# Performance work log

Hardware: AMD Instinct MI355X
Metric: run time of the kernel (lower is better)

The kernel has to match this reference:

```python
import jax, jax.numpy as jnp
import numpy as np

B, N, E, F, D = 8, 2000, 64000, 1024, 128
NEG_SLOPE = 0.01  # torch LeakyReLU default

def leaky(x):
    return jnp.where(x >= 0, x, NEG_SLOPE * x)

def gcn_conv(x, ei, W, b):
    # PyG GCNConv: add self loops, symmetric norm, x @ W, scatter-sum, + bias
    src, tgt = ei[0], ei[1]
    loops = jnp.arange(N, dtype=src.dtype)
    src_a = jnp.concatenate([src, loops])
    tgt_a = jnp.concatenate([tgt, loops])
    deg = jax.ops.segment_sum(jnp.ones(src_a.shape, x.dtype), tgt_a, num_segments=N)
    dinv = jnp.where(deg > 0, jax.lax.rsqrt(deg), 0.0)
    norm = dinv[src_a] * dinv[tgt_a]  # [E+N]
    h = x @ W                          # [N, F]
    out = jax.ops.segment_sum(norm[:, None] * h[src_a], tgt_a, num_segments=N)
    return out + b

gcn_conv_b = jax.vmap(gcn_conv, in_axes=(0, 0, None, None))

def setup_inputs() -> dict:
    key = jax.random.key(0)
    ks = jax.random.split(key, 16)
    s = lambda fan: 1.0 / np.sqrt(fan)
    return {
        "x1": jax.random.normal(ks[0], (B, N, F), jnp.float32),
        "ei1": jax.random.randint(ks[1], (B, 2, E), 0, N, jnp.int32),
        "x2": jax.random.normal(ks[2], (B, N, F), jnp.float32),
        "ei2": jax.random.randint(ks[3], (B, 2, E), 0, N, jnp.int32),
        "Wg1": jax.random.normal(ks[4], (F, F), jnp.float32) * s(F),
        "bg1": jnp.zeros((F,), jnp.float32),
        "Wf1": jax.random.normal(ks[5], (F, D), jnp.float32) * s(F),
        "bf1": jnp.zeros((D,), jnp.float32),
        "Wg2": jax.random.normal(ks[6], (F, F), jnp.float32) * s(F),
        "bg2": jnp.zeros((F,), jnp.float32),
        "Wf2": jax.random.normal(ks[7], (F, D), jnp.float32) * s(F),
        "bf2": jnp.zeros((D,), jnp.float32),
        "W1": jax.random.normal(ks[8], (2 * D, 256), jnp.float32) * s(2 * D),
        "b1": jnp.zeros((256,), jnp.float32),
        "W2": jax.random.normal(ks[9], (256, 64), jnp.float32) * s(256),
        "b2": jnp.zeros((64,), jnp.float32),
        "Wo": jax.random.normal(ks[10], (64, 1), jnp.float32) * s(64),
        "bo": jnp.zeros((1,), jnp.float32),
    }

def reference(x1, ei1, x2, ei2, Wg1, bg1, Wf1, bf1, Wg2, bg2, Wf2, bf2,
              W1, b1, W2, b2, Wo, bo):
    # branch 1
    h1 = leaky(gcn_conv_b(x1, ei1, Wg1, bg1))       # [B, N, F]
    g1 = jnp.mean(h1, axis=1)                        # [B, F]
    g1 = leaky(g1 @ Wf1 + bf1)                       # [B, D] (dropout = eval identity)
    # branch 2
    h2 = leaky(gcn_conv_b(x2, ei2, Wg2, bg2))
    g2 = jnp.mean(h2, axis=1)
    g2 = leaky(g2 @ Wf2 + bf2)
    # head
    xc = jnp.concatenate([g1, g2], axis=1)           # [B, 2D]
    xc = leaky(xc @ W1 + b1)
    xc = leaky(xc @ W2 + b2)
    return jax.nn.sigmoid(xc @ Wo + bo)              # [B, 1]
```

## Files before the change

### kernel.cpp

```cpp
#include <hip/hip_runtime.h>
#include <stdint.h>

#define B 8
#define NN 2000
#define EG 64000
#define FF 1024
#define DD 128
#define BK 32
#define NCHUNK 125

#define NB_CONV 32000
#define NB_WT   2048
#define NB_DEG  4000
#define NB_GEMMS 1024
#define NB_FILL  4000

typedef short short8 __attribute__((ext_vector_type(8)));
typedef float f32x4 __attribute__((ext_vector_type(4)));
typedef float f32x2 __attribute__((ext_vector_type(2)));

__device__ __forceinline__ unsigned short f2bf(float f) {
    union { float f; unsigned int u; } v; v.f = f;
    unsigned int u = v.u;
    unsigned int r = u + 0x7FFFu + ((u >> 16) & 1u);
    return (unsigned short)(r >> 16);
}
__device__ __forceinline__ float leaky(float v) { return v >= 0.0f ? v : 0.01f * v; }

__device__ __forceinline__ void acc8p(f32x2* __restrict__ r, float w, uint4 v) {
    union { unsigned int u; float f; } c;
    f32x2 wv = {w, w};
    f32x2 h;
    c.u = v.x << 16;          h.x = c.f;
    c.u = v.x & 0xffff0000u;  h.y = c.f;
    r[0] += wv * h;
    c.u = v.y << 16;          h.x = c.f;
    c.u = v.y & 0xffff0000u;  h.y = c.f;
    r[1] += wv * h;
    c.u = v.z << 16;          h.x = c.f;
    c.u = v.z & 0xffff0000u;  h.y = c.f;
    r[2] += wv * h;
    c.u = v.w << 16;          h.x = c.f;
    c.u = v.w & 0xffff0000u;  h.y = c.f;
    r[3] += wv * h;
}

__global__ void k_prep(const float* __restrict__ x_a, const float* __restrict__ x_b,
                       unsigned short* __restrict__ xb,
                       const float* __restrict__ Wg_a, const float* __restrict__ Wg_b,
                       unsigned short* __restrict__ wT,
                       const int* __restrict__ ei_a, const int* __restrict__ ei_b,
                       int* __restrict__ degi) {
    int blk = blockIdx.x;
    int tid = threadIdx.x;
    __shared__ float tile[32][33];
    if (blk < NB_CONV) {
        int i = blk * 256 + tid;
        float4 v = (i < NB_CONV * 128) ? ((const float4*)x_a)[i]
                                       : ((const float4*)x_b)[i - NB_CONV * 128];
        ushort4 o;
        o.x = f2bf(v.x); o.y = f2bf(v.y); o.z = f2bf(v.z); o.w = f2bf(v.w);
        ((ushort4*)xb)[i] = o;
    } else if (blk < NB_CONV + NB_WT) {
        int b2 = blk - NB_CONV;
        int z = b2 >> 10, rem = b2 & 1023;
        int by = rem >> 5, bx = rem & 31;
        int tx = tid & 31, ty = tid >> 5;
        int k0 = by * 32, n0 = bx * 32;
        const float* Wg = z ? Wg_b : Wg_a;
        unsigned short* o = wT + (size_t)z * FF * FF;
#pragma unroll
        for (int r = 0; r < 4; ++r) {
            int row = ty + r * 8;
            tile[row][tx] = Wg[(k0 + row) * FF + n0 + tx];
        }
        __syncthreads();
#pragma unroll
        for (int r = 0; r < 4; ++r) {
            int row = ty + r * 8;
            o[(n0 + row) * FF + k0 + tx] = f2bf(tile[tx][row]);
        }
    } else {
        int i = (blk - NB_CONV - NB_WT) * 256 + tid;
        int g = i / EG, e = i - g * EG;
        const int* ei = (g < B) ? (ei_a + (size_t)g * 2 * EG)
                                : (ei_b + (size_t)(g - B) * 2 * EG);
        int t = ei[EG + e];
        atomicAdd(&degi[g * NN + t], 1);
    }
}

__global__ void k_scan(const int* __restrict__ degi, int* __restrict__ csr_off,
                       int* __restrict__ cursor, float* __restrict__ dinv) {
    int g = blockIdx.x, t = threadIdx.x;
    __shared__ int part[256];
    int loc[8];
    int s = 0;
#pragma unroll
    for (int i = 0; i < 8; ++i) {
        int n = t * 8 + i;
        int c = (n < NN) ? degi[g * NN + n] : 0;
        if (n < NN) dinv[g * NN + n] = rsqrtf((float)(c + 1));
        loc[i] = s;
        s += c;
    }
    part[t] = s;
    __syncthreads();
    for (int off = 1; off < 256; off <<= 1) {
        int v = (t >= off) ? part[t - off] : 0;
        __syncthreads();
        part[t] += v;
        __syncthreads();
    }
    int base = part[t] - s;
#pragma unroll
    for (int i = 0; i < 8; ++i) {
        int n = t * 8 + i;
        if (n < NN) {
            int o = base + loc[i];
            csr_off[g * (NN + 1) + n] = o;
            cursor[g * NN + n] = o;
        }
    }
    if (t == 255) csr_off[g * (NN + 1) + NN] = part[255];
}

__launch_bounds__(256) __global__
void k_gemm_fill(const unsigned short* __restrict__ Abf, const unsigned short* __restrict__ wT,
                 unsigned short* __restrict__ Hbf,
                 const int* __restrict__ ei_a, const int* __restrict__ ei_b,
                 int* __restrict__ cursor, const float* __restrict__ dinv,
                 int2* __restrict__ epk, int nfill, int set) {
    int blk = blockIdx.x;
    __shared__ __align__(16) unsigned short As[128 * BK];
    __shared__ __align__(16) unsigned short Bs[128 * BK];
    if (blk < nfill) {
        int i = blk * 256 + threadIdx.x;
        int g = i / EG, e = i - g * EG;
        const int* ei = (g < B) ? (ei_a + (size_t)g * 2 * EG)
                                : (ei_b + (size_t)(g - B) * 2 * EG);
        int s = ei[e];
        int t = ei[EG + e];
        int pos = atomicAdd(&cursor[g * NN + t], 1);
        int2 p;
        p.x = s;
        p.y = __float_as_int(dinv[g * NN + s] * dinv[g * NN + t]);
        epk[(size_t)g * EG + pos] = p;
        return;
    }
    int b2 = blk - nfill;
    int mt = ((b2 >> 6) << 3) | (b2 & 7);
    int nt = (b2 >> 3) & 7;
    if (mt >= 125) return;
    int m0 = set * 16000 + mt * 128, n0 = nt * 128;
    const unsigned short* Bbf = wT + (size_t)set * FF * FF;

    int tid = threadIdx.x;
    int lane = tid & 63, wave = tid >> 6;
    int wr = wave >> 1, wc = wave & 1;
    int q = lane >> 4, l15 = lane & 15;
    int lr = lane >> 2, lc = lane & 3;

    f32x4 acc[4][4];
#pragma unroll
    for (int i = 0; i < 4; ++i)
#pragma unroll
        for (int j = 0; j < 4; ++j) acc[i][j] = (f32x4){0.f, 0.f, 0.f, 0.f};

    for (int kt = 0; kt < 32; ++kt) {
        int kb = kt * BK;
#pragma unroll
        for (int p = 0; p < 2; ++p) {
            int rbase = p * 64 + wave * 16;
            int r = rbase + lr;
            __builtin_amdgcn_global_load_lds(
                (const __attribute__((address_space(1))) unsigned int*)
                    &Abf[(size_t)(m0 + r) * FF + kb + lc * 8],
                (__attribute__((address_space(3))) unsigned int*)&As[rbase * BK],
                16, 0, 0);
            __builtin_amdgcn_global_load_lds(
                (const __attribute__((address_space(1))) unsigned int*)
                    &Bbf[(size_t)(n0 + r) * FF + kb + lc * 8],
                (__attribute__((address_space(3))) unsigned int*)&Bs[rbase * BK],
                16, 0, 0);
        }
        __syncthreads();
        short8 fa[4], fb[4];
#pragma unroll
        for (int i = 0; i < 4; ++i)
            fa[i] = *(const short8*)&As[(wr * 64 + i * 16 + l15) * BK + q * 8];
#pragma unroll
        for (int j = 0; j < 4; ++j)
            fb[j] = *(const short8*)&Bs[(wc * 64 + j * 16 + l15) * BK + q * 8];
#pragma unroll
        for (int i = 0; i < 4; ++i)
#pragma unroll
            for (int j = 0; j < 4; ++j)
                acc[i][j] = __builtin_amdgcn_mfma_f32_16x16x32_bf16(fa[i], fb[j], acc[i][j], 0, 0, 0);
        __syncthreads();
    }
#pragma unroll
    for (int i = 0; i < 4; ++i) {
#pragma unroll
        for (int j = 0; j < 4; ++j) {
            int n = n0 + wc * 64 + j * 16 + l15;
#pragma unroll
            for (int v = 0; v < 4; ++v) {
                int m = m0 + wr * 64 + i * 16 + q * 4 + v;
                Hbf[(size_t)m * FF + n] = f2bf(acc[i][j][v]);
            }
        }
    }
}

__launch_bounds__(256) __global__
void k_aggreduce(const unsigned short* __restrict__ Hbf, const int* __restrict__ csr_off,
                 const int2* __restrict__ epk, const float* __restrict__ dinv,
                 const float* __restrict__ bg_a, const float* __restrict__ bg_b,
                 float* __restrict__ part) {
    int blk = blockIdx.x;
    int phase = blk / 1000;
    int bp = blk - phase * 1000;
    int half = phase & 1;
    int g = (phase >> 1) * 8 + (bp & 7);
    int chunk = bp >> 3;
    int tid = threadIdx.x;
    int team = tid >> 6;
    int lane = tid & 63;
    int f0 = half * 512 + lane * 8;
    int n0 = chunk * 16 + team * 4;
    const unsigned short* Hb = Hbf + (size_t)g * NN * FF;
    const int2* ep = epk + (size_t)g * EG;
    const float* bg = (g < B) ? bg_a : bg_b;

    f32x2 bgv[4];
#pragma unroll
    for (int i = 0; i < 4; ++i) bgv[i] = (f32x2){bg[f0 + 2 * i], bg[f0 + 2 * i + 1]};
    f32x2 bsum[4];
#pragma unroll
    for (int i = 0; i < 4; ++i) bsum[i] = (f32x2){0.f, 0.f};

    for (int nn = 0; nn < 4; ++nn) {
        int n = n0 + nn;
        float dn = dinv[g * NN + n];
        int beg = csr_off[g * (NN + 1) + n];
        int end = csr_off[g * (NN + 1) + n + 1];
        f32x2 racc[4];
#pragma unroll
        for (int i = 0; i < 4; ++i) racc[i] = (f32x2){0.f, 0.f};
        {
            uint4 sv = *(const uint4*)&Hb[(n << 10) + f0];
            acc8p(racc, dn * dn, sv);
        }
        int j = beg;
        int2 pe0, pe1, pe2, pe3;
        if (j + 4 <= end) { pe0 = ep[j]; pe1 = ep[j + 1]; pe2 = ep[j + 2]; pe3 = ep[j + 3]; }
        for (; j + 8 <= end; j += 4) {
            int2 e0 = pe0, e1 = pe1, e2 = pe2, e3 = pe3;
            pe0 = ep[j + 4]; pe1 = ep[j + 5]; pe2 = ep[j + 6]; pe3 = ep[j + 7];
            uint4 v0 = *(const uint4*)&Hb[(e0.x << 10) + f0];
            uint4 v1 = *(const uint4*)&Hb[(e1.x << 10) + f0];
            uint4 v2 = *(const uint4*)&Hb[(e2.x << 10) + f0];
            uint4 v3 = *(const uint4*)&Hb[(e3.x << 10) + f0];
            acc8p(racc, __int_as_float(e0.y), v0);
            acc8p(racc, __int_as_float(e1.y), v1);
            acc8p(racc, __int_as_float(e2.y), v2);
            acc8p(racc, __int_as_float(e3.y), v3);
        }
        if (j + 4 <= end) {
            uint4 v0 = *(const uint4*)&Hb[(pe0.x << 10) + f0];
            uint4 v1 = *(const uint4*)&Hb[(pe1.x << 10) + f0];
            uint4 v2 = *(const uint4*)&Hb[(pe2.x << 10) + f0];
            uint4 v3 = *(const uint4*)&Hb[(pe3.x << 10) + f0];
            acc8p(racc, __int_as_float(pe0.y), v0);
            acc8p(racc, __int_as_float(pe1.y), v1);
            acc8p(racc, __int_as_float(pe2.y), v2);
            acc8p(racc, __int_as_float(pe3.y), v3);
            j += 4;
        }
        for (; j < end; ++j) {
            int2 e = ep[j];
            uint4 v = *(const uint4*)&Hb[(e.x << 10) + f0];
            acc8p(racc, __int_as_float(e.y), v);
        }
#pragma unroll
        for (int i = 0; i < 4; ++i) {
            f32x2 t = racc[i] + bgv[i];
            bsum[i].x += leaky(t.x);
            bsum[i].y += leaky(t.y);
        }
    }

    __shared__ float red[3][64 * 9];
    if (team > 0) {
#pragma unroll
        for (int i = 0; i < 4; ++i) {
            red[team - 1][lane * 9 + 2 * i]     = bsum[i].x;
            red[team - 1][lane * 9 + 2 * i + 1] = bsum[i].y;
        }
    }
    __syncthreads();
    if (team == 0) {
        float* o = part + ((size_t)g * NCHUNK + chunk) * FF + f0;
        float r[8];
#pragma unroll
        for (int i = 0; i < 4; ++i) {
            r[2 * i]     = bsum[i].x;
            r[2 * i + 1] = bsum[i].y;
        }
#pragma unroll
        for (int t = 0; t < 3; ++t)
#pragma unroll
            for (int i = 0; i < 8; ++i) r[i] += red[t][lane * 9 + i];
        float4 a = {r[0], r[1], r[2], r[3]};
        float4 c = {r[4], r[5], r[6], r[7]};
        *(float4*)&o[0] = a;
        *(float4*)&o[4] = c;
    }
}

__launch_bounds__(512) __global__
void k_fc(const float* __restrict__ part, const float* __restrict__ Wf_a,
          const float* __restrict__ bf_a, const float* __restrict__ Wf_b,
          const float* __restrict__ bf_b, float* __restrict__ g12) {
    int g = blockIdx.x, t = threadIdx.x;
    int d = t & 127, slice = t >> 7;
    __shared__ float gs[FF];
    __shared__ float red[4][DD];
    const float* p = part + (size_t)g * NCHUNK * FF;
#pragma unroll
    for (int i = 0; i < 2; ++i) {
        int f = i * 512 + t;
        float s = 0.f;
#pragma unroll 5
        for (int c = 0; c < NCHUNK; ++c) s += p[(size_t)c * FF + f];
        gs[f] = s;
    }
    __syncthreads();
    const float* Wf = (g < B) ? Wf_a : Wf_b;
    const float* bfv = (g < B) ? bf_a : bf_b;
    float acc = 0.f;
    int fbase = slice * 256;
#pragma unroll 8
    for (int ff = 0; ff < 256; ++ff) {
        int f = fbase + ff;
        acc += gs[f] * Wf[f * DD + d];
    }
    red[slice][d] = acc;
    __syncthreads();
    if (t < DD) {
        float a = red[0][t] + red[1][t] + red[2][t] + red[3][t];
        a = a * (1.0f / (float)NN) + bfv[t];
        g12[g * DD + t] = leaky(a);
    }
}

__launch_bounds__(256) __global__
void k_head(const float* __restrict__ g, const float* __restrict__ W1, const float* __restrict__ b1,
            const float* __restrict__ W2, const float* __restrict__ b2,
            const float* __restrict__ Wo, const float* __restrict__ bo, float* __restrict__ out) {
    __shared__ float xc[8][256];
    __shared__ float l1[8][256];
    __shared__ float l2[8][64];
    int t = threadIdx.x;
#pragma unroll
    for (int i = 0; i < 8; ++i) {
        int idx = i * 256 + t;
        int b = idx >> 8, j = idx & 255;
        xc[b][j] = (j < DD) ? g[b * DD + j] : g[B * DD + b * DD + (j - DD)];
    }
    __syncthreads();
    {
        int j = t;
        float a[8];
#pragma unroll
        for (int b = 0; b < 8; ++b) a[b] = b1[j];
        for (int k = 0; k < 256; ++k) {
            float w = W1[k * 256 + j];
#pragma unroll
            for (int b = 0; b < 8; ++b) a[b] += xc[b][k] * w;
        }
#pragma unroll
        for (int b = 0; b < 8; ++b) l1[b][j] = leaky(a[b]);
    }
    __syncthreads();
    if (t < 64) {
        int j = t;
        float a[8];
#pragma unroll
        for (int b = 0; b < 8; ++b) a[b] = b2[j];
        for (int k = 0; k < 256; ++k) {
            float w = W2[k * 64 + j];
#pragma unroll
            for (int b = 0; b < 8; ++b) a[b] += l1[b][k] * w;
        }
#pragma unroll
        for (int b = 0; b < 8; ++b) l2[b][j] = leaky(a[b]);
    }
    __syncthreads();
    if (t < 8) {
        float a = bo[0];
        for (int k = 0; k < 64; ++k) a += l2[t][k] * Wo[k];
        out[t] = 1.0f / (1.0f + expf(-a));
    }
}

extern "C" void kernel_launch(void* const* d_in, const int* in_sizes, int n_in,
                              void* d_out, int out_size, void* d_ws, size_t ws_size,
                              hipStream_t stream) {
    const float* x1  = (const float*)d_in[0];
    const int*   ei1 = (const int*)d_in[1];
    const float* x2  = (const float*)d_in[2];
    const int*   ei2 = (const int*)d_in[3];
    const float* Wg1 = (const float*)d_in[4];
    const float* bg1 = (const float*)d_in[5];
    const float* Wf1 = (const float*)d_in[6];
    const float* bf1 = (const float*)d_in[7];
    const float* Wg2 = (const float*)d_in[8];
    const float* bg2 = (const float*)d_in[9];
    const float* Wf2 = (const float*)d_in[10];
    const float* bf2 = (const float*)d_in[11];
    const float* W1  = (const float*)d_in[12];
    const float* b1  = (const float*)d_in[13];
    const float* W2  = (const float*)d_in[14];
    const float* b2  = (const float*)d_in[15];
    const float* Wo  = (const float*)d_in[16];
    const float* bo  = (const float*)d_in[17];
    float* out = (float*)d_out;

    auto align = [](size_t v) { return (v + 255) & ~(size_t)255; };
    size_t need = 0;
    size_t o_deg  = need; need += align((size_t)16 * NN * 4);
    size_t o_dinv = need; need += align((size_t)16 * NN * 4);
    size_t o_csr  = need; need += align((size_t)16 * (NN + 1) * 4);
    size_t o_cur  = need; need += align((size_t)16 * NN * 4);
    size_t o_epk  = need; need += align((size_t)16 * EG * 8);
    size_t o_xbf  = need; need += align(((size_t)16 * NN + 128) * FF * 2);
    size_t o_wT   = need; need += align((size_t)2 * FF * FF * 2);
    size_t o_hbf  = need; need += align((size_t)16 * NN * FF * 2);
    size_t o_part = need; need += align((size_t)16 * NCHUNK * FF * 4);
    size_t o_g12  = need; need += align((size_t)16 * DD * 4);
    (void)need;

    char* w = (char*)d_ws;
    int* degi    = (int*)(w + o_deg);
    float* dinv  = (float*)(w + o_dinv);
    int* csr     = (int*)(w + o_csr);
    int* cur     = (int*)(w + o_cur);
    int2* epk    = (int2*)(w + o_epk);
    unsigned short* xbf = (unsigned short*)(w + o_xbf);
    unsigned short* wT  = (unsigned short*)(w + o_wT);
    unsigned short* hbf = (unsigned short*)(w + o_hbf);
    float* part  = (float*)(w + o_part);
    float* g12   = (float*)(w + o_g12);

    hipMemsetAsync(degi, 0, (size_t)16 * NN * 4, stream);
    k_prep<<<NB_CONV + NB_WT + NB_DEG, 256, 0, stream>>>(x1, x2, xbf, Wg1, Wg2, wT,
                                                         ei1, ei2, degi);
    k_scan<<<16, 256, 0, stream>>>(degi, csr, cur, dinv);
    k_gemm_fill<<<NB_FILL + NB_GEMMS, 256, 0, stream>>>(xbf, wT, hbf, ei1, ei2, cur,
                                                        dinv, epk, NB_FILL, 0);
    k_gemm_fill<<<NB_GEMMS, 256, 0, stream>>>(xbf, wT, hbf, ei1, ei2, cur,
                                              dinv, epk, 0, 1);
    k_aggreduce<<<4000, 256, 0, stream>>>(hbf, csr, epk, dinv, bg1, bg2, part);
    k_fc<<<16, 512, 0, stream>>>(part, Wf1, bf1, Wf2, bf2, g12);
    k_head<<<1, 256, 0, stream>>>(g12, W1, b1, W2, b2, Wo, bo, out);
}
```

Measured before the change: 566.1 us.

## Overlap branch-2 GEMM with branch-1 aggregation in a combined launch

The GEMM and aggregation bodies become device functions, so one launch can hold GEMM tiles for the second graph set alongside aggregation blocks for the first set (phases 0-1). The remaining aggregation phases run in a separate launch afterwards. The first launch now puts GEMM blocks ahead of edge-fill blocks. The aim is to fill idle compute units during the memory-bound aggregation and cut launch tail gaps, at the cost of more shared memory per block in the combined kernel and possible interference between the co-running workloads.

```diff
diff --git a/kernel.cpp b/kernel.cpp
--- a/kernel.cpp
+++ b/kernel.cpp
@@ -14,6 +14,7 @@
 #define NB_DEG  4000
 #define NB_GEMMS 1024
 #define NB_FILL  4000
+#define NB_AGGH  2000
 
 typedef short short8 __attribute__((ext_vector_type(8)));
 typedef float f32x4 __attribute__((ext_vector_type(4)));
@@ -125,37 +126,16 @@
     if (t == 255) csr_off[g * (NN + 1) + NN] = part[255];
 }
 
-__launch_bounds__(256) __global__
-void k_gemm_fill(const unsigned short* __restrict__ Abf, const unsigned short* __restrict__ wT,
-                 unsigned short* __restrict__ Hbf,
-                 const int* __restrict__ ei_a, const int* __restrict__ ei_b,
-                 int* __restrict__ cursor, const float* __restrict__ dinv,
-                 int2* __restrict__ epk, int nfill, int set) {
-    int blk = blockIdx.x;
-    __shared__ __align__(16) unsigned short As[128 * BK];
-    __shared__ __align__(16) unsigned short Bs[128 * BK];
-    if (blk < nfill) {
-        int i = blk * 256 + threadIdx.x;
-        int g = i / EG, e = i - g * EG;
-        const int* ei = (g < B) ? (ei_a + (size_t)g * 2 * EG)
-                                : (ei_b + (size_t)(g - B) * 2 * EG);
-        int s = ei[e];
-        int t = ei[EG + e];
-        int pos = atomicAdd(&cursor[g * NN + t], 1);
-        int2 p;
-        p.x = s;
-        p.y = __float_as_int(dinv[g * NN + s] * dinv[g * NN + t]);
-        epk[(size_t)g * EG + pos] = p;
-        return;
-    }
-    int b2 = blk - nfill;
+__device__ __forceinline__ void gemm_body(int b2, int set,
+        const unsigned short* __restrict__ Abf, const unsigned short* __restrict__ wT,
+        unsigned short* __restrict__ Hbf, int tid,
+        unsigned short* As, unsigned short* Bs) {
     int mt = ((b2 >> 6) << 3) | (b2 & 7);
     int nt = (b2 >> 3) & 7;
     if (mt >= 125) return;
     int m0 = set * 16000 + mt * 128, n0 = nt * 128;
     const unsigned short* Bbf = wT + (size_t)set * FF * FF;
 
-    int tid = threadIdx.x;
     int lane = tid & 63, wave = tid >> 6;
     int wr = wave >> 1, wc = wave & 1;
     int q = lane >> 4, l15 = lane & 15;
@@ -213,18 +193,14 @@
     }
 }
 
-__launch_bounds__(256) __global__
-void k_aggreduce(const unsigned short* __restrict__ Hbf, const int* __restrict__ csr_off,
-                 const int2* __restrict__ epk, const float* __restrict__ dinv,
-                 const float* __restrict__ bg_a, const float* __restrict__ bg_b,
-                 float* __restrict__ part) {
-    int blk = blockIdx.x;
-    int phase = blk / 1000;
-    int bp = blk - phase * 1000;
+__device__ __forceinline__ void agg_body(int bp, int phase,
+        const unsigned short* __restrict__ Hbf, const int* __restrict__ csr_off,
+        const int2* __restrict__ epk, const float* __restrict__ dinv,
+        const float* __restrict__ bg_a, const float* __restrict__ bg_b,
+        float* __restrict__ part, int tid, float* red ) {
     int half = phase & 1;
     int g = (phase >> 1) * 8 + (bp & 7);
     int chunk = bp >> 3;
-    int tid = threadIdx.x;
     int team = tid >> 6;
     int lane = tid & 63;
     int f0 = half * 512 + lane * 8;
@@ -291,12 +267,11 @@
         }
     }
 
-    __shared__ float red[3][64 * 9];
     if (team > 0) {
 #pragma unroll
         for (int i = 0; i < 4; ++i) {
-            red[team - 1][lane * 9 + 2 * i]     = bsum[i].x;
-            red[team - 1][lane * 9 + 2 * i + 1] = bsum[i].y;
+            red[(team - 1) * 576 + lane * 9 + 2 * i]     = bsum[i].x;
+            red[(team - 1) * 576 + lane * 9 + 2 * i + 1] = bsum[i].y;
         }
     }
     __syncthreads();
@@ -311,12 +286,71 @@
 #pragma unroll
         for (int t = 0; t < 3; ++t)
 #pragma unroll
-            for (int i = 0; i < 8; ++i) r[i] += red[t][lane * 9 + i];
+            for (int i = 0; i < 8; ++i) r[i] += red[t * 576 + lane * 9 + i];
         float4 a = {r[0], r[1], r[2], r[3]};
         float4 c = {r[4], r[5], r[6], r[7]};
         *(float4*)&o[0] = a;
         *(float4*)&o[4] = c;
     }
+}
+
+__launch_bounds__(256) __global__
+void k_gemm_fill(const unsigned short* __restrict__ Abf, const unsigned short* __restrict__ wT,
+                 unsigned short* __restrict__ Hbf,
+                 const int* __restrict__ ei_a, const int* __restrict__ ei_b,
+                 int* __restrict__ cursor, const float* __restrict__ dinv,
+                 int2* __restrict__ epk) {
+    int blk = blockIdx.x;
+    __shared__ __align__(16) unsigned short As[128 * BK];
+    __shared__ __align__(16) unsigned short Bs[128 * BK];
+    if (blk < NB_GEMMS) {
+        gemm_body(blk, 0, Abf, wT, Hbf, threadIdx.x, As, Bs);
+        return;
+    }
+    int i = (blk - NB_GEMMS) * 256 + threadIdx.x;
+    int g = i / EG, e = i - g * EG;
+    const int* ei = (g < B) ? (ei_a + (size_t)g * 2 * EG)
+                            : (ei_b + (size_t)(g - B) * 2 * EG);
+    int s = ei[e];
+    int t = ei[EG + e];
+    int pos = atomicAdd(&cursor[g * NN + t], 1);
+    int2 p;
+    p.x = s;
+    p.y = __float_as_int(dinv[g * NN + s] * dinv[g * NN + t]);
+    epk[(size_t)g * EG + pos] = p;
+}
+
+__launch_bounds__(256) __global__
+void k_gemm_agg(const unsigned short* __restrict__ Abf, const unsigned short* __restrict__ wT,
+                unsigned short* __restrict__ Hbf,
+                const int* __restrict__ csr_off, const int2* __restrict__ epk,
+                const float* __restrict__ dinv,
+                const float* __restrict__ bg_a, const float* __restrict__ bg_b,
+                float* __restrict__ part) {
+    int blk = blockIdx.x;
+    __shared__ __align__(16) unsigned short As[128 * BK];
+    __shared__ __align__(16) unsigned short Bs[128 * BK];
+    __shared__ float red[3 * 576];
+    if (blk < NB_GEMMS) {
+        gemm_body(blk, 1, Abf, wT, Hbf, threadIdx.x, As, Bs);
+        return;
+    }
+    int bp2 = blk - NB_GEMMS;
+    int phase = bp2 / 1000;
+    int bp = bp2 - phase * 1000;
+    agg_body(bp, phase, Hbf, csr_off, epk, dinv, bg_a, bg_b, part, threadIdx.x, red);
+}
+
+__launch_bounds__(256) __global__
+void k_agg2(const unsigned short* __restrict__ Hbf, const int* __restrict__ csr_off,
+            const int2* __restrict__ epk, const float* __restrict__ dinv,
+            const float* __restrict__ bg_a, const float* __restrict__ bg_b,
+            float* __restrict__ part) {
+    int blk = blockIdx.x;
+    __shared__ float red[3 * 576];
+    int phase = 2 + blk / 1000;
+    int bp = blk - (phase - 2) * 1000;
+    agg_body(bp, phase, Hbf, csr_off, epk, dinv, bg_a, bg_b, part, threadIdx.x, red);
 }
 
 __launch_bounds__(512) __global__
@@ -458,11 +492,11 @@
     k_prep<<<NB_CONV + NB_WT + NB_DEG, 256, 0, stream>>>(x1, x2, xbf, Wg1, Wg2, wT,
                                                          ei1, ei2, degi);
     k_scan<<<16, 256, 0, stream>>>(degi, csr, cur, dinv);
-    k_gemm_fill<<<NB_FILL + NB_GEMMS, 256, 0, stream>>>(xbf, wT, hbf, ei1, ei2, cur,
-                                                        dinv, epk, NB_FILL, 0);
-    k_gemm_fill<<<NB_GEMMS, 256, 0, stream>>>(xbf, wT, hbf, ei1, ei2, cur,
-                                              dinv, epk, 0, 1);
-    k_aggreduce<<<4000, 256, 0, stream>>>(hbf, csr, epk, dinv, bg1, bg2, part);
+    k_gemm_fill<<<NB_GEMMS + NB_FILL, 256, 0, stream>>>(xbf, wT, hbf, ei1, ei2, cur,
+                                                        dinv, epk);
+    k_gemm_agg<<<NB_GEMMS + NB_AGGH, 256, 0, stream>>>(xbf, wT, hbf, csr, epk, dinv,
+                                                       bg1, bg2, part);
+    k_agg2<<<NB_AGGH, 256, 0, stream>>>(hbf, csr, epk, dinv, bg1, bg2, part);
     k_fc<<<16, 512, 0, stream>>>(part, Wf1, bf1, Wf2, bf2, g12);
     k_head<<<1, 256, 0, stream>>>(g12, W1, b1, W2, b2, Wo, bo, out);
 }
```

Result: no change. 568.3 us (+0.4%).
